# Performance work log

Hardware: AMD Instinct MI355X
Metric: run time of the kernel (lower is better)

The kernel has to match this reference:

```python
import jax, jax.numpy as jnp
import numpy as np

N = 50_000      # nodes
E = 800_000     # edges
IN_NF = 16      # input/output node feature dim
H = 64          # hidden_nf
NB = 2          # n_layers (EquivariantBlocks)
NG = 2          # inv_sublayers (GCLs per block)
NORM_FACTOR = 100.0
NORM_CONST = 1.0
EDGE_IN = 2 * H + 2  # edges_in_d = 2 (current + initial squared distance)


def setup_inputs() -> dict:
    key = jax.random.key(0)
    ks = iter(jax.random.split(key, 32))
    rn = lambda s: jax.random.normal(next(ks), s, dtype=jnp.float32)
    lin = lambda s: rn(s) / np.sqrt(s[-2]).astype(np.float32)  # ~xavier-ish
    inp = {
        'h': rn((N, IN_NF)),
        'x': rn((N, 3)),
        'row': jax.random.randint(next(ks), (E,), 0, N, dtype=jnp.int32),
        'col': jax.random.randint(next(ks), (E,), 0, N, dtype=jnp.int32),
        # embedding in/out
        'emb_w': lin((IN_NF, H)), 'emb_b': jnp.zeros((H,), jnp.float32),
        'out_w': lin((H, IN_NF)), 'out_b': jnp.zeros((IN_NF,), jnp.float32),
        # 4 GCLs total (NB*NG), stacked on leading axis
        'e_w1': lin((NB * NG, EDGE_IN, H)), 'e_b1': jnp.zeros((NB * NG, H), jnp.float32),
        'e_w2': lin((NB * NG, H, H)),       'e_b2': jnp.zeros((NB * NG, H), jnp.float32),
        'n_w1': lin((NB * NG, 2 * H, H)),   'n_b1': jnp.zeros((NB * NG, H), jnp.float32),
        'n_w2': lin((NB * NG, H, H)),       'n_b2': jnp.zeros((NB * NG, H), jnp.float32),
        # 2 EquivariantUpdates (one per block)
        'q_w1': lin((NB, EDGE_IN, H)), 'q_b1': jnp.zeros((NB, H), jnp.float32),
        'q_w2': lin((NB, H, H)),       'q_b2': jnp.zeros((NB, H), jnp.float32),
        'q_w3': lin((NB, H, 1)) * 0.001,  # xavier gain=0.001, no bias
    }
    return inp


def _egnn(h, x, row, col, emb_w, emb_b, out_w, out_b,
          e_w1, e_b1, e_w2, e_b2, n_w1, n_b1, n_w2, n_b2,
          q_w1, q_b1, q_w2, q_b2, q_w3):
    def coord2diff(xc):
        d = xc[row] - xc[col]                      # [E,3]
        radial = jnp.sum(d * d, axis=1, keepdims=True)  # [E,1]
        d = d / (jnp.sqrt(radial + 1e-8) + NORM_CONST)
        return radial, d

    dist0, _ = coord2diff(x)                       # initial distances, passed to every block
    h = h @ emb_w + emb_b
    for b in range(NB):
        radial, coord_diff = coord2diff(x)
        edge_attr = jnp.concatenate([radial, dist0], axis=1)  # [E,2]
        for i in range(NG):
            l = b * NG + i
            inp = jnp.concatenate([h[row], h[col], edge_attr], axis=1)  # [E, 2H+2]
            mij = jax.nn.silu(jax.nn.silu(inp @ e_w1[l] + e_b1[l]) @ e_w2[l] + e_b2[l])
            agg = jax.ops.segment_sum(mij, row, num_segments=N) / NORM_FACTOR
            node_in = jnp.concatenate([h, agg], axis=1)                 # [N, 2H]
            h = h + jax.nn.silu(node_in @ n_w1[l] + n_b1[l]) @ n_w2[l] + n_b2[l]
        # equivariant coordinate update
        inp = jnp.concatenate([h[row], h[col], edge_attr], axis=1)
        phi = jax.nn.silu(jax.nn.silu(inp @ q_w1[b] + q_b1[b]) @ q_w2[b] + q_b2[b]) @ q_w3[b]  # [E,1]
        trans = coord_diff * phi
        x = x + jax.ops.segment_sum(trans, row, num_segments=N) / NORM_FACTOR
    h = h @ out_w + out_b
    return h, x


def reference(h, x, row, col, emb_w, emb_b, out_w, out_b,
              e_w1, e_b1, e_w2, e_b2, n_w1, n_b1, n_w2, n_b2,
              q_w1, q_b1, q_w2, q_b2, q_w3):
    return _egnn(h, x, row, col, emb_w, emb_b, out_w, out_b,
                 e_w1, e_b1, e_w2, e_b2, n_w1, n_b1, n_w2, n_b2,
                 q_w1, q_b1, q_w2, q_b2, q_w3)
```

## Files before the change

kernel.cpp:

```cpp
#include <hip/hip_runtime.h>

#define NN 50000
#define NE 800000
#define NB 196

typedef unsigned int  u32;
typedef unsigned short u16;
typedef __attribute__((ext_vector_type(8))) short short8;
typedef __attribute__((ext_vector_type(4))) float f32x4;

union ABfrag { uint2 u2[2]; uint4 u4; short8 s8; };

__device__ __forceinline__ float silu_f(float v) {
    return v * __builtin_amdgcn_rcpf(1.0f + __expf(-v));
}
__device__ __forceinline__ u32 pk2(float lo, float hi) {
    return __builtin_amdgcn_perm(__float_as_uint(hi) + 0x8000u,
                                 __float_as_uint(lo) + 0x8000u, 0x07060302u);
}
__device__ __forceinline__ float bff(u32 h) { return __uint_as_float(h << 16); }

__global__ __launch_bounds__(256, 4) void k_embed(const float* __restrict__ h,
        const float* __restrict__ w, const float* __restrict__ b,
        float* __restrict__ h64) {
    int n = blockIdx.x * 256 + threadIdx.x;
    if (n >= NN) return;
    const float4* h4 = (const float4*)(h + (long)n * 16);
    float in[16];
    #pragma unroll
    for (int c = 0; c < 4; ++c) {
        float4 v = h4[c];
        in[4*c+0] = v.x; in[4*c+1] = v.y; in[4*c+2] = v.z; in[4*c+3] = v.w;
    }
    float acc[64];
    #pragma unroll
    for (int j = 0; j < 64; ++j) acc[j] = b[j];
    #pragma unroll
    for (int k = 0; k < 16; ++k) {
        #pragma unroll
        for (int j = 0; j < 64; ++j) acc[j] = fmaf(in[k], w[k*64 + j], acc[j]);
    }
    float4* o4 = (float4*)(h64 + (long)n * 64);
    #pragma unroll
    for (int c = 0; c < 16; ++c)
        o4[c] = make_float4(acc[4*c+0], acc[4*c+1], acc[4*c+2], acc[4*c+3]);
}

__global__ __launch_bounds__(256, 4) void k_hist(const int* __restrict__ row,
        int* __restrict__ deg) {
    int e = blockIdx.x * 256 + threadIdx.x;
    if (e < NE) atomicAdd(&deg[row[e]], 1);
}

__global__ __launch_bounds__(256, 4) void k_scanA(const int* __restrict__ deg,
        int* __restrict__ bsum) {
    int t = threadIdx.x, i = blockIdx.x * 256 + t;
    int v = (i < NN) ? deg[i] : 0;
    #pragma unroll
    for (int d = 1; d < 64; d <<= 1) v += __shfl_xor(v, d);
    __shared__ int ws[4];
    if ((t & 63) == 0) ws[t >> 6] = v;
    __syncthreads();
    if (t == 0) bsum[blockIdx.x] = ws[0] + ws[1] + ws[2] + ws[3];
}

__global__ __launch_bounds__(256) void k_scanB(const int* __restrict__ bsum,
        int* __restrict__ bpre) {
    __shared__ int s[256];
    int t = threadIdx.x;
    int v = (t < NB) ? bsum[t] : 0;
    s[t] = v;
    __syncthreads();
    #pragma unroll
    for (int d = 1; d < 256; d <<= 1) {
        int u = (t >= d) ? s[t - d] : 0;
        __syncthreads();
        s[t] += u;
        __syncthreads();
    }
    if (t < NB) bpre[t] = s[t] - v;
}

__global__ __launch_bounds__(256, 4) void k_scanC(const int* __restrict__ deg,
        const int* __restrict__ bpre, int* __restrict__ base) {
    int t = threadIdx.x, i = blockIdx.x * 256 + t;
    int lane = t & 63, w = t >> 6;
    int v = (i < NN) ? deg[i] : 0;
    int x = v;
    #pragma unroll
    for (int d = 1; d < 64; d <<= 1) {
        int u = __shfl_up(x, d);
        if (lane >= d) x += u;
    }
    __shared__ int wsum[4];
    if (lane == 63) wsum[w] = x;
    __syncthreads();
    int off = bpre[blockIdx.x];
    #pragma unroll
    for (int ww = 0; ww < 3; ++ww) if (ww < w) off += wsum[ww];
    if (i < NN) base[i] = off + x - v;
}

__global__ __launch_bounds__(256, 4) void k_scatter(const int* __restrict__ row,
        const int* __restrict__ col, int* __restrict__ base,
        int* __restrict__ rowS, int* __restrict__ colS) {
    int e = blockIdx.x * 256 + threadIdx.x;
    if (e >= NE) return;
    int r = row[e];
    int p = atomicAdd(&base[r], 1);
    rowS[p] = r;
    colS[p] = col[e];
}

__global__ __launch_bounds__(256, 4) void k_radial(const float* __restrict__ x,
        const int* __restrict__ rowS, const int* __restrict__ colS,
        float* __restrict__ radial) {
    int e = blockIdx.x * 256 + threadIdx.x;
    if (e >= NE) return;
    int r = rowS[e], c = colS[e];
    float dx = x[r*3+0] - x[c*3+0];
    float dy = x[r*3+1] - x[c*3+1];
    float dz = x[r*3+2] - x[c*3+2];
    radial[e] = dx*dx + dy*dy + dz*dz;
}

__device__ __forceinline__ u32 bfr_rne(float x) {
    u32 u = __float_as_uint(x);
    u += 0x7fffu + ((u >> 16) & 1u);
    return u >> 16;
}
__global__ __launch_bounds__(256, 4) void k_wconv(const float* __restrict__ e_w2,
        const float* __restrict__ q_w2, const float* __restrict__ n_w1,
        const float* __restrict__ n_w2, const float* __restrict__ e_w1,
        const float* __restrict__ q_w1, u16* __restrict__ wf) {
    int t = blockIdx.x * 256 + threadIdx.x;
    if (t >= 122880) return;
    int j, lane, n, s, k, col;
    if (t < 24576) {
        int L = t >> 12, v = t & 4095;
        j = v & 7; lane = (v >> 3) & 63; int ns = v >> 9; n = ns >> 1; s = ns & 1;
        k = 8*(lane >> 4) + j + 32*s;
        col = 16*n + (lane & 15);
        const float* src = (L < 4) ? e_w2 + (size_t)L*4096 : q_w2 + (size_t)(L-4)*4096;
        wf[t] = (u16)bfr_rne(src[k*64 + col]);
    } else if (t < 57344) {
        int u = t - 24576; int L = u >> 13, v = u & 8191;
        j = v & 7; lane = (v >> 3) & 63; int ns = v >> 9; n = ns >> 2; s = ns & 3;
        k = 8*(lane >> 4) + j + 32*s;
        col = 16*n + (lane & 15);
        wf[t] = (u16)bfr_rne(n_w1[(size_t)L*8192 + k*64 + col]);
    } else if (t < 73728) {
        int u = t - 57344; int L = u >> 12, v = u & 4095;
        j = v & 7; lane = (v >> 3) & 63; int ns = v >> 9; n = ns >> 1; s = ns & 1;
        k = 8*(lane >> 4) + j + 32*s;
        col = 16*n + (lane & 15);
        wf[t] = (u16)bfr_rne(n_w2[(size_t)L*4096 + k*64 + col]);
    } else {
        int u = t - 73728;
        int L = u >> 13;
        int v = u & 8191;
        int m = v >> 12;
        int v2 = v & 4095;
        j = v2 & 7; lane = (v2 >> 3) & 63; int ns = v2 >> 9; n = ns >> 1; s = ns & 1;
        k = 8*(lane >> 4) + j + 32*s;
        col = 16*n + (lane & 15);
        const float* src = (L < 4) ? e_w1 + (size_t)L*130*64
                                   : q_w1 + (size_t)(L-4)*130*64;
        wf[t] = (u16)bfr_rne(src[(size_t)(m*64 + k)*64 + col]);
    }
}

__global__ __launch_bounds__(256, 4) void k_pq(const float* __restrict__ h64,
        const u16* __restrict__ wpf, const float* __restrict__ b1,
        u32* __restrict__ Pb, u32* __restrict__ Qb) {
    __shared__ u16 A[64*64];
    __shared__ u16 XP[64*68], XQ[64*68];
    int t = threadIdx.x, w = t >> 6, lane = t & 63;
    int nb0 = blockIdx.x * 64;
    #pragma unroll
    for (int i = 0; i < 4; ++i) {
        int idx = i*256 + t;
        int r = idx >> 4, c = idx & 15;
        int n = nb0 + r;
        float4 v = make_float4(0.f, 0.f, 0.f, 0.f);
        if (n < NN) v = ((const float4*)(h64 + (size_t)n*64))[c];
        uint2 pk = make_uint2(pk2(v.x, v.y), pk2(v.z, v.w));
        *(uint2*)((char*)A + r*128 + ((8*c) ^ ((r & 15) << 3))) = pk;
    }
    __syncthreads();
    int r0 = lane & 15, g = lane >> 4;
    ABfrag bp[2], bq[2];
    #pragma unroll
    for (int s = 0; s < 2; ++s) {
        bp[s].u4 = *(const uint4*)(wpf + ((size_t)(w*2 + s)*64 + lane)*8);
        bq[s].u4 = *(const uint4*)(wpf + 4096 + ((size_t)(w*2 + s)*64 + lane)*8);
    }
    f32x4 aP[4], aQ[4];
    #pragma unroll
    for (int t4 = 0; t4 < 4; ++t4) {
        aP[t4] = (f32x4){0.f, 0.f, 0.f, 0.f};
        aQ[t4] = (f32x4){0.f, 0.f, 0.f, 0.f};
    }
    #pragma unroll
    for (int t4 = 0; t4 < 4; ++t4) {
        #pragma unroll
        for (int s = 0; s < 2; ++s) {
            int boff = 16*g + 64*s;
            ABfrag af;
            af.u2[0] = *(uint2*)((char*)A + (16*t4 + r0)*128 + ( boff      ^ (r0 << 3)));
            af.u2[1] = *(uint2*)((char*)A + (16*t4 + r0)*128 + ((boff + 8) ^ (r0 << 3)));
            aP[t4] = __builtin_amdgcn_mfma_f32_16x16x32_bf16(af.s8, bp[s].s8, aP[t4], 0, 0, 0);
            aQ[t4] = __builtin_amdgcn_mfma_f32_16x16x32_bf16(af.s8, bq[s].s8, aQ[t4], 0, 0, 0);
        }
    }
    float bv = b1[16*w + r0];
    #pragma unroll
    for (int t4 = 0; t4 < 4; ++t4)
        #pragma unroll
        for (int q = 0; q < 4; ++q) {
            int rw = 16*t4 + 4*g + q;
            XP[rw*68 + 16*w + r0] = (u16)(pk2(aP[t4][q] + bv, 0.f) & 0xffffu);
            XQ[rw*68 + 16*w + r0] = (u16)(pk2(aQ[t4][q], 0.f) & 0xffffu);
        }
    __syncthreads();
    int node = t >> 2, part = t & 3;
    if (nb0 + node < NN) {
        const u32* XPw = (const u32*)XP;
        const u32* XQw = (const u32*)XQ;
        u32 b[8];
        #pragma unroll
        for (int j = 0; j < 8; ++j) b[j] = XPw[node*34 + 8*part + j];
        uint4* dp = (uint4*)(Pb + (size_t)(nb0 + node)*32 + part*8);
        dp[0] = make_uint4(b[0], b[1], b[2], b[3]);
        dp[1] = make_uint4(b[4], b[5], b[6], b[7]);
        #pragma unroll
        for (int j = 0; j < 8; ++j) b[j] = XQw[node*34 + 8*part + j];
        uint4* dq = (uint4*)(Qb + (size_t)(nb0 + node)*32 + part*8);
        dq[0] = make_uint4(b[0], b[1], b[2], b[3]);
        dq[1] = make_uint4(b[4], b[5], b[6], b[7]);
    }
}

__global__ __launch_bounds__(256, 4) void k_edge(
        const u32* __restrict__ Pb, const u32* __restrict__ Qb,
        const float* __restrict__ radial, const float* __restrict__ dist0,
        const int* __restrict__ rowS, const int* __restrict__ colS,
        const float* __restrict__ w1t, const u16* __restrict__ w2f,
        const float* __restrict__ b2, float* __restrict__ agg) {
    __shared__ u16 M_lds[4][64*66];
    int tid = threadIdx.x;
    int w = tid >> 6, lane = tid & 63;
    int ebase = blockIdx.x * 256 + w * 64;
    u16* Mw = M_lds[w];
    int r0 = lane & 15, g = lane >> 4;
    float wa[16], wb[16];
    *(float4*)&wa[0]  = *(const float4*)(w1t + 8*g);
    *(float4*)&wa[4]  = *(const float4*)(w1t + 8*g + 4);
    *(float4*)&wa[8]  = *(const float4*)(w1t + 32 + 8*g);
    *(float4*)&wa[12] = *(const float4*)(w1t + 36 + 8*g);
    *(float4*)&wb[0]  = *(const float4*)(w1t + 64 + 8*g);
    *(float4*)&wb[4]  = *(const float4*)(w1t + 68 + 8*g);
    *(float4*)&wb[8]  = *(const float4*)(w1t + 96 + 8*g);
    *(float4*)&wb[12] = *(const float4*)(w1t + 100 + 8*g);
    ABfrag bf[4][2];
    #pragma unroll
    for (int n = 0; n < 4; ++n)
        #pragma unroll
        for (int s = 0; s < 2; ++s)
            bf[n][s].u4 = *(const uint4*)(w2f + ((n*2 + s)*64 + lane)*8);
    float b2v[4];
    #pragma unroll
    for (int n = 0; n < 4; ++n) b2v[n] = b2[16*n + r0];
    #pragma unroll
    for (int t = 0; t < 4; ++t) {
        int et = ebase + 16*t + r0;
        int r = rowS[et], c = colS[et];
        float rad = radial[et], d0 = dist0[et];
        uint4 pA = *(const uint4*)(Pb + (size_t)r*32 + 4*g);
        uint4 pB = *(const uint4*)(Pb + (size_t)r*32 + 16 + 4*g);
        uint4 qA = *(const uint4*)(Qb + (size_t)c*32 + 4*g);
        uint4 qB = *(const uint4*)(Qb + (size_t)c*32 + 16 + 4*g);
        u32 pu[8] = {pA.x, pA.y, pA.z, pA.w, pB.x, pB.y, pB.z, pB.w};
        u32 qu[8] = {qA.x, qA.y, qA.z, qA.w, qB.x, qB.y, qB.z, qB.w};
        u32 pk[8];
        #pragma unroll
        for (int i = 0; i < 8; ++i) {
            int kb = (i >> 2) * 8 + (i & 3) * 2;
            float pl = bff(pu[i] & 0xffffu), ph = bff(pu[i] >> 16);
            float ql = bff(qu[i] & 0xffffu), qh = bff(qu[i] >> 16);
            float h0 = silu_f(pl + ql + rad*wa[kb]   + d0*wb[kb]);
            float h1 = silu_f(ph + qh + rad*wa[kb+1] + d0*wb[kb+1]);
            pk[i] = pk2(h0, h1);
        }
        ABfrag af0, af1;
        af0.u4 = make_uint4(pk[0], pk[1], pk[2], pk[3]);
        af1.u4 = make_uint4(pk[4], pk[5], pk[6], pk[7]);
        f32x4 acc[4];
        #pragma unroll
        for (int n = 0; n < 4; ++n) acc[n] = (f32x4){0.f, 0.f, 0.f, 0.f};
        #pragma unroll
        for (int n = 0; n < 4; ++n) {
            acc[n] = __builtin_amdgcn_mfma_f32_16x16x32_bf16(af0.s8, bf[n][0].s8, acc[n], 0, 0, 0);
            acc[n] = __builtin_amdgcn_mfma_f32_16x16x32_bf16(af1.s8, bf[n][1].s8, acc[n], 0, 0, 0);
        }
        #pragma unroll
        for (int n = 0; n < 4; ++n) {
            f32x4 z = acc[n];
            u32 m0 = pk2(silu_f(z[0] + b2v[n]), silu_f(z[1] + b2v[n]));
            u32 m1 = pk2(silu_f(z[2] + b2v[n]), silu_f(z[3] + b2v[n]));
            *(uint2*)((char*)Mw + (16*n + r0)*132 + 32*t + 8*g) = make_uint2(m0, m1);
        }
    }
    int rl = rowS[ebase + lane];
    int rnext = __shfl_down(rl, 1);
    unsigned long long tm = __ballot((lane == 63) || (rnext != rl));
    float racc = 0.0f;
    #pragma unroll
    for (int ch = 0; ch < 16; ++ch) {
        uint2 mm = *(uint2*)((char*)Mw + lane*132 + 8*ch);
        u32 mw[2] = {mm.x, mm.y};
        #pragma unroll
        for (int q = 0; q < 4; ++q) {
            int ee = 4*ch + q;
            racc += bff((mw[q >> 1] >> ((q & 1) * 16)) & 0xffffu);
            if ((tm >> ee) & 1ull) {
                int rr = __builtin_amdgcn_readlane(rl, ee);
                atomicAdd(&agg[(size_t)rr*64 + lane], racc);
                racc = 0.0f;
            }
        }
    }
}

__global__ __launch_bounds__(256, 3) void k_node_pq(float* __restrict__ h64,
        const float* __restrict__ agg,
        const u16* __restrict__ w1f, const float* __restrict__ b1,
        const u16* __restrict__ w2f, const float* __restrict__ b2,
        const u16* __restrict__ wpf, const float* __restrict__ b1pq,
        u32* __restrict__ Pb, u32* __restrict__ Qb) {
    __shared__ u16 S[16512];
    u16* A0 = S;
    u16* A1 = S + 4096;
    u16* H  = S + 8192;
    u16* D  = S + 12288;
    u16* An = S;
    u16* XPh = S + 4096;
    u16* XQh = S + 8448;
    int t = threadIdx.x, w = t >> 6, lane = t & 63;
    int nb0 = blockIdx.x * 64;
    #pragma unroll
    for (int i = 0; i < 8; ++i) {
        int idx = i*256 + t;
        int r = idx >> 5, c = idx & 31;
        int n = nb0 + r;
        float4 v = make_float4(0.f, 0.f, 0.f, 0.f);
        if (n < NN) {
            if (c < 16) v = ((const float4*)(h64 + (size_t)n*64))[c];
            else {
                float4 a = ((const float4*)(agg + (size_t)n*64))[c-16];
                v = make_float4(a.x*0.01f, a.y*0.01f, a.z*0.01f, a.w*0.01f);
            }
        }
        uint2 pk = make_uint2(pk2(v.x, v.y), pk2(v.z, v.w));
        u16* dst = (c < 16) ? A0 : A1;
        int cc = c & 15;
        *(uint2*)((char*)dst + r*128 + ((8*cc) ^ ((r & 15) << 3))) = pk;
    }
    __syncthreads();
    int r0 = lane & 15, g = lane >> 4;
    ABfrag bf1[4];
    #pragma unroll
    for (int s = 0; s < 4; ++s)
        bf1[s].u4 = *(const uint4*)(w1f + ((size_t)(w*4 + s)*64 + lane)*8);
    f32x4 acc[4];
    #pragma unroll
    for (int t4 = 0; t4 < 4; ++t4) acc[t4] = (f32x4){0.f, 0.f, 0.f, 0.f};
    #pragma unroll
    for (int t4 = 0; t4 < 4; ++t4) {
        #pragma unroll
        for (int s = 0; s < 4; ++s) {
            const u16* Ah = (s < 2) ? A0 : A1;
            int boff = 16*g + 64*(s & 1);
            ABfrag af;
            af.u2[0] = *(uint2*)((char*)Ah + (16*t4 + r0)*128 + ( boff      ^ (r0 << 3)));
            af.u2[1] = *(uint2*)((char*)Ah + (16*t4 + r0)*128 + ((boff + 8) ^ (r0 << 3)));
            acc[t4] = __builtin_amdgcn_mfma_f32_16x16x32_bf16(
                af.s8, bf1[s].s8, acc[t4], 0, 0, 0);
        }
    }
    float b1v = b1[16*w + r0];
    #pragma unroll
    for (int t4 = 0; t4 < 4; ++t4)
        #pragma unroll
        for (int q = 0; q < 4; ++q) {
            int rw = 16*t4 + 4*g + q;
            u16 hv = (u16)(pk2(silu_f(acc[t4][q] + b1v), 0.f) & 0xffffu);
            *(u16*)((char*)H + rw*128 + ((2*(16*w + r0)) ^ ((rw & 15) << 3))) = hv;
        }
    __syncthreads();
    ABfrag bf2[2];
    #pragma unroll
    for (int s = 0; s < 2; ++s)
        bf2[s].u4 = *(const uint4*)(w2f + ((size_t)(w*2 + s)*64 + lane)*8);
    f32x4 acc2[4];
    #pragma unroll
    for (int t4 = 0; t4 < 4; ++t4) acc2[t4] = (f32x4){0.f, 0.f, 0.f, 0.f};
    #pragma unroll
    for (int t4 = 0; t4 < 4; ++t4) {
        #pragma unroll
        for (int s = 0; s < 2; ++s) {
            int boff = 16*g + 64*s;
            ABfrag af;
            af.u2[0] = *(uint2*)((char*)H + (16*t4 + r0)*128 + ( boff      ^ (r0 << 3)));
            af.u2[1] = *(uint2*)((char*)H + (16*t4 + r0)*128 + ((boff + 8) ^ (r0 << 3)));
            acc2[t4] = __builtin_amdgcn_mfma_f32_16x16x32_bf16(
                af.s8, bf2[s].s8, acc2[t4], 0, 0, 0);
        }
    }
    float b2v = b2[16*w + r0];
    #pragma unroll
    for (int t4 = 0; t4 < 4; ++t4)
        #pragma unroll
        for (int q = 0; q < 4; ++q) {
            int rw = 16*t4 + 4*g + q;
            D[rw*66 + 16*w + r0] = (u16)(pk2(acc2[t4][q] + b2v, 0.f) & 0xffffu);
        }
    __syncthreads();
    #pragma unroll
    for (int i = 0; i < 4; ++i) {
        int idx = i*256 + t;
        int rr = idx >> 4, cc = idx & 15;
        int n = nb0 + rr;
        float4 v = make_float4(0.f, 0.f, 0.f, 0.f);
        if (n < NN) {
            v = ((const float4*)(h64 + (size_t)n*64))[cc];
            v.x += bff(D[rr*66 + 4*cc + 0]);
            v.y += bff(D[rr*66 + 4*cc + 1]);
            v.z += bff(D[rr*66 + 4*cc + 2]);
            v.w += bff(D[rr*66 + 4*cc + 3]);
            ((float4*)(h64 + (size_t)n*64))[cc] = v;
        }
        uint2 pk = make_uint2(pk2(v.x, v.y), pk2(v.z, v.w));
        *(uint2*)((char*)An + rr*128 + ((8*cc) ^ ((rr & 15) << 3))) = pk;
    }
    __syncthreads();
    ABfrag bp[2], bq[2];
    #pragma unroll
    for (int s = 0; s < 2; ++s) {
        bp[s].u4 = *(const uint4*)(wpf + ((size_t)(w*2 + s)*64 + lane)*8);
        bq[s].u4 = *(const uint4*)(wpf + 4096 + ((size_t)(w*2 + s)*64 + lane)*8);
    }
    f32x4 aP[4], aQ[4];
    #pragma unroll
    for (int t4 = 0; t4 < 4; ++t4) {
        aP[t4] = (f32x4){0.f, 0.f, 0.f, 0.f};
        aQ[t4] = (f32x4){0.f, 0.f, 0.f, 0.f};
    }
    #pragma unroll
    for (int t4 = 0; t4 < 4; ++t4) {
        #pragma unroll
        for (int s = 0; s < 2; ++s) {
            int boff = 16*g + 64*s;
            ABfrag af;
            af.u2[0] = *(uint2*)((char*)An + (16*t4 + r0)*128 + ( boff      ^ (r0 << 3)));
            af.u2[1] = *(uint2*)((char*)An + (16*t4 + r0)*128 + ((boff + 8) ^ (r0 << 3)));
            aP[t4] = __builtin_amdgcn_mfma_f32_16x16x32_bf16(af.s8, bp[s].s8, aP[t4], 0, 0, 0);
            aQ[t4] = __builtin_amdgcn_mfma_f32_16x16x32_bf16(af.s8, bq[s].s8, aQ[t4], 0, 0, 0);
        }
    }
    float bv = b1pq[16*w + r0];
    #pragma unroll
    for (int t4 = 0; t4 < 4; ++t4)
        #pragma unroll
        for (int q = 0; q < 4; ++q) {
            int rw = 16*t4 + 4*g + q;
            XPh[rw*68 + 16*w + r0] = (u16)(pk2(aP[t4][q] + bv, 0.f) & 0xffffu);
            XQh[rw*68 + 16*w + r0] = (u16)(pk2(aQ[t4][q], 0.f) & 0xffffu);
        }
    __syncthreads();
    int node = t >> 2, part = t & 3;
    if (nb0 + node < NN) {
        const u32* XPw = (const u32*)XPh;
        const u32* XQw = (const u32*)XQh;
        u32 b[8];
        #pragma unroll
        for (int j = 0; j < 8; ++j) b[j] = XPw[node*34 + 8*part + j];
        uint4* dp = (uint4*)(Pb + (size_t)(nb0 + node)*32 + part*8);
        dp[0] = make_uint4(b[0], b[1], b[2], b[3]);
        dp[1] = make_uint4(b[4], b[5], b[6], b[7]);
        #pragma unroll
        for (int j = 0; j < 8; ++j) b[j] = XQw[node*34 + 8*part + j];
        uint4* dq = (uint4*)(Qb + (size_t)(nb0 + node)*32 + part*8);
        dq[0] = make_uint4(b[0], b[1], b[2], b[3]);
        dq[1] = make_uint4(b[4], b[5], b[6], b[7]);
    }
}

__global__ __launch_bounds__(256, 4) void k_coord(
        const u32* __restrict__ Pb, const u32* __restrict__ Qb,
        const float* __restrict__ radial, const float* __restrict__ dist0,
        const int* __restrict__ rowS, const int* __restrict__ colS,
        const float* __restrict__ w1t, const u16* __restrict__ w2f,
        const float* __restrict__ b2, const float* __restrict__ w3,
        const float* __restrict__ x_old, float* __restrict__ x_new) {
    __shared__ float PHL[4][64];
    int tid = threadIdx.x;
    int w = tid >> 6, lane = tid & 63;
    int ebase = blockIdx.x * 256 + w * 64;
    int r0 = lane & 15, g = lane >> 4;
    float wa[16], wb[16];
    *(float4*)&wa[0]  = *(const float4*)(w1t + 8*g);
    *(float4*)&wa[4]  = *(const float4*)(w1t + 8*g + 4);
    *(float4*)&wa[8]  = *(const float4*)(w1t + 32 + 8*g);
    *(float4*)&wa[12] = *(const float4*)(w1t + 36 + 8*g);
    *(float4*)&wb[0]  = *(const float4*)(w1t + 64 + 8*g);
    *(float4*)&wb[4]  = *(const float4*)(w1t + 68 + 8*g);
    *(float4*)&wb[8]  = *(const float4*)(w1t + 96 + 8*g);
    *(float4*)&wb[12] = *(const float4*)(w1t + 100 + 8*g);
    ABfrag bf[4][2];
    #pragma unroll
    for (int n = 0; n < 4; ++n)
        #pragma unroll
        for (int s = 0; s < 2; ++s)
            bf[n][s].u4 = *(const uint4*)(w2f + ((n*2 + s)*64 + lane)*8);
    float w3v[4], b2v[4];
    #pragma unroll
    for (int n = 0; n < 4; ++n) { w3v[n] = w3[16*n + r0]; b2v[n] = b2[16*n + r0]; }
    float ph[16];
    #pragma unroll
    for (int t = 0; t < 4; ++t) {
        int et = ebase + 16*t + r0;
        int r = rowS[et], c = colS[et];
        float rad = radial[et], d0 = dist0[et];
        uint4 pA = *(const uint4*)(Pb + (size_t)r*32 + 4*g);
        uint4 pB = *(const uint4*)(Pb + (size_t)r*32 + 16 + 4*g);
        uint4 qA = *(const uint4*)(Qb + (size_t)c*32 + 4*g);
        uint4 qB = *(const uint4*)(Qb + (size_t)c*32 + 16 + 4*g);
        u32 pu[8] = {pA.x, pA.y, pA.z, pA.w, pB.x, pB.y, pB.z, pB.w};
        u32 qu[8] = {qA.x, qA.y, qA.z, qA.w, qB.x, qB.y, qB.z, qB.w};
        u32 pk[8];
        #pragma unroll
        for (int i = 0; i < 8; ++i) {
            int kb = (i >> 2) * 8 + (i & 3) * 2;
            float pl = bff(pu[i] & 0xffffu), phh = bff(pu[i] >> 16);
            float ql = bff(qu[i] & 0xffffu), qh = bff(qu[i] >> 16);
            float h0 = silu_f(pl + ql + rad*wa[kb]   + d0*wb[kb]);
            float h1 = silu_f(phh + qh + rad*wa[kb+1] + d0*wb[kb+1]);
            pk[i] = pk2(h0, h1);
        }
        ABfrag af0, af1;
        af0.u4 = make_uint4(pk[0], pk[1], pk[2], pk[3]);
        af1.u4 = make_uint4(pk[4], pk[5], pk[6], pk[7]);
        f32x4 acc[4];
        #pragma unroll
        for (int n = 0; n < 4; ++n) acc[n] = (f32x4){0.f, 0.f, 0.f, 0.f};
        #pragma unroll
        for (int n = 0; n < 4; ++n) {
            acc[n] = __builtin_amdgcn_mfma_f32_16x16x32_bf16(af0.s8, bf[n][0].s8, acc[n], 0, 0, 0);
            acc[n] = __builtin_amdgcn_mfma_f32_16x16x32_bf16(af1.s8, bf[n][1].s8, acc[n], 0, 0, 0);
        }
        #pragma unroll
        for (int q = 0; q < 4; ++q) {
            float s = 0.f;
            #pragma unroll
            for (int n = 0; n < 4; ++n)
                s = fmaf(silu_f(acc[n][q] + b2v[n]), w3v[n], s);
            ph[t*4 + q] = s;
        }
    }
    #pragma unroll
    for (int d = 1; d < 16; d <<= 1)
        #pragma unroll
        for (int i = 0; i < 16; ++i) ph[i] += __shfl_xor(ph[i], d);
    if (r0 == 0) {
        #pragma unroll
        for (int t = 0; t < 4; ++t)
            #pragma unroll
            for (int q = 0; q < 4; ++q)
                PHL[w][16*t + 4*g + q] = ph[t*4 + q];
    }
    int e = ebase + lane;
    float phi = PHL[w][lane] * 0.01f;
    int r = rowS[e], c = colS[e];
    float rad = radial[e];
    float dx = x_old[r*3+0] - x_old[c*3+0];
    float dy = x_old[r*3+1] - x_old[c*3+1];
    float dz = x_old[r*3+2] - x_old[c*3+2];
    float inv = phi / (sqrtf(rad + 1e-8f) + 1.0f);
    float tx = dx * inv, ty = dy * inv, tz = dz * inv;
    int rprev = __shfl_up(r, 1);
    bool head = (lane == 0) || (rprev != r);
    unsigned long long hm = __ballot(head);
    int runid = __popcll(hm & ((2ull << lane) - 1ull));
    #pragma unroll
    for (int d = 1; d < 64; d <<= 1) {
        float ox = __shfl_up(tx, d);
        float oy = __shfl_up(ty, d);
        float oz = __shfl_up(tz, d);
        int orid = __shfl_up(runid, d);
        if (lane >= d && orid == runid) { tx += ox; ty += oy; tz += oz; }
    }
    int rid_next = __shfl_down(runid, 1);
    bool tail = (lane == 63) || (rid_next != runid);
    if (tail) {
        atomicAdd(&x_new[r*3+0], tx);
        atomicAdd(&x_new[r*3+1], ty);
        atomicAdd(&x_new[r*3+2], tz);
    }
}

__global__ __launch_bounds__(256, 4) void k_out(const float* __restrict__ h64,
        const float* __restrict__ w, const float* __restrict__ b,
        float* __restrict__ out) {
    int n = blockIdx.x * 256 + threadIdx.x;
    if (n >= NN) return;
    float acc[16];
    #pragma unroll
    for (int j = 0; j < 16; ++j) acc[j] = b[j];
    const float4* h4 = (const float4*)(h64 + (long)n*64);
    #pragma unroll
    for (int c = 0; c < 16; ++c) {
        float4 v = h4[c];
        float vv[4] = {v.x, v.y, v.z, v.w};
        #pragma unroll
        for (int t = 0; t < 4; ++t) {
            #pragma unroll
            for (int j = 0; j < 16; ++j)
                acc[j] = fmaf(vv[t], w[(4*c+t)*16 + j], acc[j]);
        }
    }
    float4* o4 = (float4*)(out + (long)n*16);
    #pragma unroll
    for (int cq = 0; cq < 4; ++cq)
        o4[cq] = make_float4(acc[4*cq+0],acc[4*cq+1],acc[4*cq+2],acc[4*cq+3]);
}

extern "C" void kernel_launch(void* const* d_in, const int* in_sizes, int n_in,
                              void* d_out, int out_size, void* d_ws, size_t ws_size,
                              hipStream_t stream) {
    const float* h_in  = (const float*)d_in[0];
    const float* x_in  = (const float*)d_in[1];
    const int*   row   = (const int*)d_in[2];
    const int*   col   = (const int*)d_in[3];
    const float* emb_w = (const float*)d_in[4];
    const float* emb_b = (const float*)d_in[5];
    const float* out_w = (const float*)d_in[6];
    const float* out_b = (const float*)d_in[7];
    const float* e_w1  = (const float*)d_in[8];
    const float* e_b1  = (const float*)d_in[9];
    const float* e_w2  = (const float*)d_in[10];
    const float* e_b2  = (const float*)d_in[11];
    const float* n_w1  = (const float*)d_in[12];
    const float* n_b1  = (const float*)d_in[13];
    const float* n_w2  = (const float*)d_in[14];
    const float* n_b2  = (const float*)d_in[15];
    const float* q_w1  = (const float*)d_in[16];
    const float* q_b1  = (const float*)d_in[17];
    const float* q_w2  = (const float*)d_in[18];
    const float* q_b2  = (const float*)d_in[19];
    const float* q_w3  = (const float*)d_in[20];

    const size_t WF_N = 122880;
    const size_t WF_BYTES = WF_N * sizeof(u16);
    size_t need = WF_BYTES + ((size_t)NN*64*4 + (size_t)NE*2 + (size_t)NN*3
                   + (size_t)NE*2 + (size_t)NN*2 + 1024) * sizeof(float);
    if (ws_size < need) return;

    u16*   wf    = (u16*)d_ws;
    float* fb    = (float*)((char*)d_ws + WF_BYTES);
    float* h64   = fb;
    u32*   Pb    = (u32*)(h64 + (size_t)NN*64);
    u32*   Qb    = Pb + (size_t)NN*32;
    float* agg   = (float*)(Qb + (size_t)NN*32);
    float* d0S   = agg   + (size_t)NN*64;
    float* radS  = d0S   + (size_t)NE;
    float* xA    = radS  + (size_t)NE;
    int*   rowS  = (int*)(xA + (size_t)NN*3);
    int*   colS  = rowS  + (size_t)NE;
    int*   deg   = colS  + (size_t)NE;
    int*   base  = deg   + (size_t)NN;
    int*   bsum  = base  + (size_t)NN;
    int*   bpre  = bsum  + 256;

    float* out_h = (float*)d_out;
    float* out_x = out_h + (size_t)NN*16;

    dim3 th(256);
    dim3 nb((NN + 255)/256);
    dim3 eb(NE/256);
    dim3 t64b((NN + 63)/64);

    hipMemsetAsync(deg, 0, (size_t)NN*sizeof(int), stream);
    k_hist<<<eb, th, 0, stream>>>(row, deg);
    k_scanA<<<NB, th, 0, stream>>>(deg, bsum);
    k_scanB<<<1, th, 0, stream>>>(bsum, bpre);
    k_scanC<<<NB, th, 0, stream>>>(deg, bpre, base);
    k_scatter<<<eb, th, 0, stream>>>(row, col, base, rowS, colS);
    k_wconv<<<480, th, 0, stream>>>(e_w2, q_w2, n_w1, n_w2, e_w1, q_w1, wf);

    k_radial<<<eb, th, 0, stream>>>(x_in, rowS, colS, d0S);
    k_embed<<<nb, th, 0, stream>>>(h_in, emb_w, emb_b, h64);

    const u16* nw1f = wf + 24576;
    const u16* nw2f = wf + 57344;
    const u16* pqf  = wf + 73728;

    for (int b = 0; b < 2; ++b) {
        const float* x_old;
        float*       x_new;
        const float* radp;
        if (b == 0) {
            x_old = x_in;  x_new = xA;    radp = d0S;
        } else {
            x_old = xA;    x_new = out_x; radp = radS;
            k_radial<<<eb, th, 0, stream>>>(x_old, rowS, colS, radS);
        }
        for (int i = 0; i < 2; ++i) {
            int l = b*2 + i;
            if (i == 0)
                k_pq<<<t64b, th, 0, stream>>>(h64, pqf + (size_t)l*8192,
                                              e_b1 + (size_t)l*64, Pb, Qb);
            hipMemsetAsync(agg, 0, (size_t)NN*64*sizeof(float), stream);
            k_edge<<<eb, th, 0, stream>>>(Pb, Qb, radp, d0S, rowS, colS,
                    e_w1 + (size_t)l*130*64 + 128*64,
                    wf + (size_t)l*4096,
                    e_b2 + (size_t)l*64, agg);
            const u16* nxt_f  = (i == 0) ? pqf + (size_t)(l+1)*8192
                                         : pqf + (size_t)(4 + b)*8192;
            const float* nxt_b = (i == 0) ? e_b1 + (size_t)(l+1)*64
                                          : q_b1 + (size_t)b*64;
            k_node_pq<<<t64b, th, 0, stream>>>(h64, agg,
                    nw1f + (size_t)l*8192, n_b1 + (size_t)l*64,
                    nw2f + (size_t)l*4096, n_b2 + (size_t)l*64,
                    nxt_f, nxt_b, Pb, Qb);
        }
        hipMemcpyAsync(x_new, x_old, (size_t)NN*3*sizeof(float),
                       hipMemcpyDeviceToDevice, stream);
        k_coord<<<eb, th, 0, stream>>>(Pb, Qb, radp, d0S, rowS, colS,
                q_w1 + (size_t)b*130*64 + 128*64,
                wf + (size_t)(4 + b)*4096,
                q_b2 + (size_t)b*64, q_w3 + (size_t)b*64, x_old, x_new);
    }
    k_out<<<nb, th, 0, stream>>>(h64, out_w, out_b, out_h);
}
```

Before: 668.8 us.

## Pack edge records, zero agg in node kernel, fuse next block's PQ projection

Edge row, col, initial distance and current radial are packed into one int4 record per sorted edge, so edge and coord kernels issue a single 16-byte load instead of four scalar loads. The node kernel now zeroes agg after reading it, which removes the per-layer memset. The last node kernel of block 0 also computes the P/Q projections for block 1's first GCL into a second buffer, which removes a separate k_pq launch. The host loop is unrolled explicitly, and the cost is extra workspace for the second P/Q buffers plus the unused padding in each edge record.

```diff
diff --git a/kernel.cpp b/kernel.cpp
--- a/kernel.cpp
+++ b/kernel.cpp
@@ -103,25 +103,27 @@
 
 __global__ __launch_bounds__(256, 4) void k_scatter(const int* __restrict__ row,
         const int* __restrict__ col, int* __restrict__ base,
-        int* __restrict__ rowS, int* __restrict__ colS) {
+        int4* __restrict__ erec) {
     int e = blockIdx.x * 256 + threadIdx.x;
     if (e >= NE) return;
     int r = row[e];
     int p = atomicAdd(&base[r], 1);
-    rowS[p] = r;
-    colS[p] = col[e];
+    erec[p] = make_int4(r, col[e], 0, 0);
 }
 
 __global__ __launch_bounds__(256, 4) void k_radial(const float* __restrict__ x,
-        const int* __restrict__ rowS, const int* __restrict__ colS,
-        float* __restrict__ radial) {
+        int4* __restrict__ erec, int mode) {
     int e = blockIdx.x * 256 + threadIdx.x;
     if (e >= NE) return;
-    int r = rowS[e], c = colS[e];
+    int4 rec = erec[e];
+    int r = rec.x, c = rec.y;
     float dx = x[r*3+0] - x[c*3+0];
     float dy = x[r*3+1] - x[c*3+1];
     float dz = x[r*3+2] - x[c*3+2];
-    radial[e] = dx*dx + dy*dy + dz*dz;
+    float rad = dx*dx + dy*dy + dz*dz;
+    rec.w = __float_as_int(rad);
+    if (mode == 0) rec.z = rec.w;
+    erec[e] = rec;
 }
 
 __device__ __forceinline__ u32 bfr_rne(float x) {
@@ -243,8 +245,7 @@
 
 __global__ __launch_bounds__(256, 4) void k_edge(
         const u32* __restrict__ Pb, const u32* __restrict__ Qb,
-        const float* __restrict__ radial, const float* __restrict__ dist0,
-        const int* __restrict__ rowS, const int* __restrict__ colS,
+        const int4* __restrict__ erec,
         const float* __restrict__ w1t, const u16* __restrict__ w2f,
         const float* __restrict__ b2, float* __restrict__ agg) {
     __shared__ u16 M_lds[4][64*66];
@@ -274,8 +275,9 @@
     #pragma unroll
     for (int t = 0; t < 4; ++t) {
         int et = ebase + 16*t + r0;
-        int r = rowS[et], c = colS[et];
-        float rad = radial[et], d0 = dist0[et];
+        int4 rec = erec[et];
+        int r = rec.x, c = rec.y;
+        float d0 = __int_as_float(rec.z), rad = __int_as_float(rec.w);
         uint4 pA = *(const uint4*)(Pb + (size_t)r*32 + 4*g);
         uint4 pB = *(const uint4*)(Pb + (size_t)r*32 + 16 + 4*g);
         uint4 qA = *(const uint4*)(Qb + (size_t)c*32 + 4*g);
@@ -311,7 +313,7 @@
             *(uint2*)((char*)Mw + (16*n + r0)*132 + 32*t + 8*g) = make_uint2(m0, m1);
         }
     }
-    int rl = rowS[ebase + lane];
+    int rl = *(const int*)(erec + ebase + lane);
     int rnext = __shfl_down(rl, 1);
     unsigned long long tm = __ballot((lane == 63) || (rnext != rl));
     float racc = 0.0f;
@@ -333,11 +335,13 @@
 }
 
 __global__ __launch_bounds__(256, 3) void k_node_pq(float* __restrict__ h64,
-        const float* __restrict__ agg,
+        float* __restrict__ agg,
         const u16* __restrict__ w1f, const float* __restrict__ b1,
         const u16* __restrict__ w2f, const float* __restrict__ b2,
         const u16* __restrict__ wpf, const float* __restrict__ b1pq,
-        u32* __restrict__ Pb, u32* __restrict__ Qb) {
+        u32* __restrict__ Pb, u32* __restrict__ Qb,
+        const u16* __restrict__ wpf2, const float* __restrict__ b1pq2,
+        u32* __restrict__ Pb2, u32* __restrict__ Qb2, int has2) {
     __shared__ u16 S[16512];
     u16* A0 = S;
     u16* A1 = S + 4096;
@@ -358,6 +362,7 @@
             if (c < 16) v = ((const float4*)(h64 + (size_t)n*64))[c];
             else {
                 float4 a = ((const float4*)(agg + (size_t)n*64))[c-16];
+                ((float4*)(agg + (size_t)n*64))[c-16] = make_float4(0.f,0.f,0.f,0.f);
                 v = make_float4(a.x*0.01f, a.y*0.01f, a.z*0.01f, a.w*0.01f);
             }
         }
@@ -444,62 +449,68 @@
         *(uint2*)((char*)An + rr*128 + ((8*cc) ^ ((rr & 15) << 3))) = pk;
     }
     __syncthreads();
-    ABfrag bp[2], bq[2];
-    #pragma unroll
-    for (int s = 0; s < 2; ++s) {
-        bp[s].u4 = *(const uint4*)(wpf + ((size_t)(w*2 + s)*64 + lane)*8);
-        bq[s].u4 = *(const uint4*)(wpf + 4096 + ((size_t)(w*2 + s)*64 + lane)*8);
-    }
-    f32x4 aP[4], aQ[4];
-    #pragma unroll
-    for (int t4 = 0; t4 < 4; ++t4) {
-        aP[t4] = (f32x4){0.f, 0.f, 0.f, 0.f};
-        aQ[t4] = (f32x4){0.f, 0.f, 0.f, 0.f};
-    }
-    #pragma unroll
-    for (int t4 = 0; t4 < 4; ++t4) {
+    for (int set = 0; set < 1 + (has2 ? 1 : 0); ++set) {
+        const u16* wp = set ? wpf2 : wpf;
+        const float* bb = set ? b1pq2 : b1pq;
+        u32* Pd = set ? Pb2 : Pb;
+        u32* Qd = set ? Qb2 : Qb;
+        ABfrag bp[2], bq[2];
         #pragma unroll
         for (int s = 0; s < 2; ++s) {
-            int boff = 16*g + 64*s;
-            ABfrag af;
-            af.u2[0] = *(uint2*)((char*)An + (16*t4 + r0)*128 + ( boff      ^ (r0 << 3)));
-            af.u2[1] = *(uint2*)((char*)An + (16*t4 + r0)*128 + ((boff + 8) ^ (r0 << 3)));
-            aP[t4] = __builtin_amdgcn_mfma_f32_16x16x32_bf16(af.s8, bp[s].s8, aP[t4], 0, 0, 0);
-            aQ[t4] = __builtin_amdgcn_mfma_f32_16x16x32_bf16(af.s8, bq[s].s8, aQ[t4], 0, 0, 0);
-        }
-    }
-    float bv = b1pq[16*w + r0];
-    #pragma unroll
-    for (int t4 = 0; t4 < 4; ++t4)
-        #pragma unroll
-        for (int q = 0; q < 4; ++q) {
-            int rw = 16*t4 + 4*g + q;
-            XPh[rw*68 + 16*w + r0] = (u16)(pk2(aP[t4][q] + bv, 0.f) & 0xffffu);
-            XQh[rw*68 + 16*w + r0] = (u16)(pk2(aQ[t4][q], 0.f) & 0xffffu);
-        }
-    __syncthreads();
-    int node = t >> 2, part = t & 3;
-    if (nb0 + node < NN) {
-        const u32* XPw = (const u32*)XPh;
-        const u32* XQw = (const u32*)XQh;
-        u32 b[8];
-        #pragma unroll
-        for (int j = 0; j < 8; ++j) b[j] = XPw[node*34 + 8*part + j];
-        uint4* dp = (uint4*)(Pb + (size_t)(nb0 + node)*32 + part*8);
-        dp[0] = make_uint4(b[0], b[1], b[2], b[3]);
-        dp[1] = make_uint4(b[4], b[5], b[6], b[7]);
-        #pragma unroll
-        for (int j = 0; j < 8; ++j) b[j] = XQw[node*34 + 8*part + j];
-        uint4* dq = (uint4*)(Qb + (size_t)(nb0 + node)*32 + part*8);
-        dq[0] = make_uint4(b[0], b[1], b[2], b[3]);
-        dq[1] = make_uint4(b[4], b[5], b[6], b[7]);
+            bp[s].u4 = *(const uint4*)(wp + ((size_t)(w*2 + s)*64 + lane)*8);
+            bq[s].u4 = *(const uint4*)(wp + 4096 + ((size_t)(w*2 + s)*64 + lane)*8);
+        }
+        f32x4 aP[4], aQ[4];
+        #pragma unroll
+        for (int t4 = 0; t4 < 4; ++t4) {
+            aP[t4] = (f32x4){0.f, 0.f, 0.f, 0.f};
+            aQ[t4] = (f32x4){0.f, 0.f, 0.f, 0.f};
+        }
+        #pragma unroll
+        for (int t4 = 0; t4 < 4; ++t4) {
+            #pragma unroll
+            for (int s = 0; s < 2; ++s) {
+                int boff = 16*g + 64*s;
+                ABfrag af;
+                af.u2[0] = *(uint2*)((char*)An + (16*t4 + r0)*128 + ( boff      ^ (r0 << 3)));
+                af.u2[1] = *(uint2*)((char*)An + (16*t4 + r0)*128 + ((boff + 8) ^ (r0 << 3)));
+                aP[t4] = __builtin_amdgcn_mfma_f32_16x16x32_bf16(af.s8, bp[s].s8, aP[t4], 0, 0, 0);
+                aQ[t4] = __builtin_amdgcn_mfma_f32_16x16x32_bf16(af.s8, bq[s].s8, aQ[t4], 0, 0, 0);
+            }
+        }
+        float bv = bb[16*w + r0];
+        #pragma unroll
+        for (int t4 = 0; t4 < 4; ++t4)
+            #pragma unroll
+            for (int q = 0; q < 4; ++q) {
+                int rw = 16*t4 + 4*g + q;
+                XPh[rw*68 + 16*w + r0] = (u16)(pk2(aP[t4][q] + bv, 0.f) & 0xffffu);
+                XQh[rw*68 + 16*w + r0] = (u16)(pk2(aQ[t4][q], 0.f) & 0xffffu);
+            }
+        __syncthreads();
+        int node = t >> 2, part = t & 3;
+        if (nb0 + node < NN) {
+            const u32* XPw = (const u32*)XPh;
+            const u32* XQw = (const u32*)XQh;
+            u32 b[8];
+            #pragma unroll
+            for (int j = 0; j < 8; ++j) b[j] = XPw[node*34 + 8*part + j];
+            uint4* dp = (uint4*)(Pd + (size_t)(nb0 + node)*32 + part*8);
+            dp[0] = make_uint4(b[0], b[1], b[2], b[3]);
+            dp[1] = make_uint4(b[4], b[5], b[6], b[7]);
+            #pragma unroll
+            for (int j = 0; j < 8; ++j) b[j] = XQw[node*34 + 8*part + j];
+            uint4* dq = (uint4*)(Qd + (size_t)(nb0 + node)*32 + part*8);
+            dq[0] = make_uint4(b[0], b[1], b[2], b[3]);
+            dq[1] = make_uint4(b[4], b[5], b[6], b[7]);
+        }
+        __syncthreads();
     }
 }
 
 __global__ __launch_bounds__(256, 4) void k_coord(
         const u32* __restrict__ Pb, const u32* __restrict__ Qb,
-        const float* __restrict__ radial, const float* __restrict__ dist0,
-        const int* __restrict__ rowS, const int* __restrict__ colS,
+        const int4* __restrict__ erec,
         const float* __restrict__ w1t, const u16* __restrict__ w2f,
         const float* __restrict__ b2, const float* __restrict__ w3,
         const float* __restrict__ x_old, float* __restrict__ x_new) {
@@ -530,8 +541,9 @@
     #pragma unroll
     for (int t = 0; t < 4; ++t) {
         int et = ebase + 16*t + r0;
-        int r = rowS[et], c = colS[et];
-        float rad = radial[et], d0 = dist0[et];
+        int4 rec = erec[et];
+        int r = rec.x, c = rec.y;
+        float d0 = __int_as_float(rec.z), rad = __int_as_float(rec.w);
         uint4 pA = *(const uint4*)(Pb + (size_t)r*32 + 4*g);
         uint4 pB = *(const uint4*)(Pb + (size_t)r*32 + 16 + 4*g);
         uint4 qA = *(const uint4*)(Qb + (size_t)c*32 + 4*g);
@@ -581,8 +593,9 @@
     }
     int e = ebase + lane;
     float phi = PHL[w][lane] * 0.01f;
-    int r = rowS[e], c = colS[e];
-    float rad = radial[e];
+    int4 rec = erec[e];
+    int r = rec.x, c = rec.y;
+    float rad = __int_as_float(rec.w);
     float dx = x_old[r*3+0] - x_old[c*3+0];
     float dy = x_old[r*3+1] - x_old[c*3+1];
     float dz = x_old[r*3+2] - x_old[c*3+2];
@@ -662,25 +675,24 @@
 
     const size_t WF_N = 122880;
     const size_t WF_BYTES = WF_N * sizeof(u16);
-    size_t need = WF_BYTES + ((size_t)NN*64*4 + (size_t)NE*2 + (size_t)NN*3
-                   + (size_t)NE*2 + (size_t)NN*2 + 1024) * sizeof(float);
+    size_t need = WF_BYTES + ((size_t)NN*64 + (size_t)NN*32*4 + (size_t)NN*64
+                   + (size_t)NE*4 + (size_t)NN*3 + (size_t)NN*2 + 2048) * 4;
     if (ws_size < need) return;
 
     u16*   wf    = (u16*)d_ws;
     float* fb    = (float*)((char*)d_ws + WF_BYTES);
     float* h64   = fb;
     u32*   Pb    = (u32*)(h64 + (size_t)NN*64);
-    u32*   Qb    = Pb + (size_t)NN*32;
-    float* agg   = (float*)(Qb + (size_t)NN*32);
-    float* d0S   = agg   + (size_t)NN*64;
-    float* radS  = d0S   + (size_t)NE;
-    float* xA    = radS  + (size_t)NE;
-    int*   rowS  = (int*)(xA + (size_t)NN*3);
-    int*   colS  = rowS  + (size_t)NE;
-    int*   deg   = colS  + (size_t)NE;
-    int*   base  = deg   + (size_t)NN;
-    int*   bsum  = base  + (size_t)NN;
-    int*   bpre  = bsum  + 256;
+    u32*   Qb    = Pb  + (size_t)NN*32;
+    u32*   Pb2   = Qb  + (size_t)NN*32;
+    u32*   Qb2   = Pb2 + (size_t)NN*32;
+    float* agg   = (float*)(Qb2 + (size_t)NN*32);
+    int4*  erec  = (int4*)(agg + (size_t)NN*64);
+    float* xA    = (float*)(erec + (size_t)NE);
+    int*   deg   = (int*)(xA + (size_t)NN*3);
+    int*   base  = deg  + (size_t)NN;
+    int*   bsum  = base + (size_t)NN;
+    int*   bpre  = bsum + 256;
 
     float* out_h = (float*)d_out;
     float* out_x = out_h + (size_t)NN*16;
@@ -695,51 +707,55 @@
     k_scanA<<<NB, th, 0, stream>>>(deg, bsum);
     k_scanB<<<1, th, 0, stream>>>(bsum, bpre);
     k_scanC<<<NB, th, 0, stream>>>(deg, bpre, base);
-    k_scatter<<<eb, th, 0, stream>>>(row, col, base, rowS, colS);
+    k_scatter<<<eb, th, 0, stream>>>(row, col, base, erec);
     k_wconv<<<480, th, 0, stream>>>(e_w2, q_w2, n_w1, n_w2, e_w1, q_w1, wf);
 
-    k_radial<<<eb, th, 0, stream>>>(x_in, rowS, colS, d0S);
+    k_radial<<<eb, th, 0, stream>>>(x_in, erec, 0);
     k_embed<<<nb, th, 0, stream>>>(h_in, emb_w, emb_b, h64);
+    hipMemsetAsync(agg, 0, (size_t)NN*64*sizeof(float), stream);
 
     const u16* nw1f = wf + 24576;
     const u16* nw2f = wf + 57344;
     const u16* pqf  = wf + 73728;
 
-    for (int b = 0; b < 2; ++b) {
-        const float* x_old;
-        float*       x_new;
-        const float* radp;
-        if (b == 0) {
-            x_old = x_in;  x_new = xA;    radp = d0S;
-        } else {
-            x_old = xA;    x_new = out_x; radp = radS;
-            k_radial<<<eb, th, 0, stream>>>(x_old, rowS, colS, radS);
-        }
-        for (int i = 0; i < 2; ++i) {
-            int l = b*2 + i;
-            if (i == 0)
-                k_pq<<<t64b, th, 0, stream>>>(h64, pqf + (size_t)l*8192,
-                                              e_b1 + (size_t)l*64, Pb, Qb);
-            hipMemsetAsync(agg, 0, (size_t)NN*64*sizeof(float), stream);
-            k_edge<<<eb, th, 0, stream>>>(Pb, Qb, radp, d0S, rowS, colS,
-                    e_w1 + (size_t)l*130*64 + 128*64,
-                    wf + (size_t)l*4096,
-                    e_b2 + (size_t)l*64, agg);
-            const u16* nxt_f  = (i == 0) ? pqf + (size_t)(l+1)*8192
-                                         : pqf + (size_t)(4 + b)*8192;
-            const float* nxt_b = (i == 0) ? e_b1 + (size_t)(l+1)*64
-                                          : q_b1 + (size_t)b*64;
-            k_node_pq<<<t64b, th, 0, stream>>>(h64, agg,
-                    nw1f + (size_t)l*8192, n_b1 + (size_t)l*64,
-                    nw2f + (size_t)l*4096, n_b2 + (size_t)l*64,
-                    nxt_f, nxt_b, Pb, Qb);
-        }
-        hipMemcpyAsync(x_new, x_old, (size_t)NN*3*sizeof(float),
-                       hipMemcpyDeviceToDevice, stream);
-        k_coord<<<eb, th, 0, stream>>>(Pb, Qb, radp, d0S, rowS, colS,
-                q_w1 + (size_t)b*130*64 + 128*64,
-                wf + (size_t)(4 + b)*4096,
-                q_b2 + (size_t)b*64, q_w3 + (size_t)b*64, x_old, x_new);
-    }
+    k_pq<<<t64b, th, 0, stream>>>(h64, pqf, e_b1, Pb, Qb);
+    k_edge<<<eb, th, 0, stream>>>(Pb, Qb, erec,
+            e_w1 + 128*64, wf, e_b2, agg);
+    k_node_pq<<<t64b, th, 0, stream>>>(h64, agg,
+            nw1f, n_b1, nw2f, n_b2,
+            pqf + 8192, e_b1 + 64, Pb, Qb,
+            nullptr, nullptr, nullptr, nullptr, 0);
+    k_edge<<<eb, th, 0, stream>>>(Pb, Qb, erec,
+            e_w1 + (size_t)1*130*64 + 128*64, wf + 4096, e_b2 + 64, agg);
+    k_node_pq<<<t64b, th, 0, stream>>>(h64, agg,
+            nw1f + 8192, n_b1 + 64, nw2f + 4096, n_b2 + 64,
+            pqf + (size_t)4*8192, q_b1, Pb, Qb,
+            pqf + (size_t)2*8192, e_b1 + 128, Pb2, Qb2, 1);
+    hipMemcpyAsync(xA, x_in, (size_t)NN*3*sizeof(float),
+                   hipMemcpyDeviceToDevice, stream);
+    k_coord<<<eb, th, 0, stream>>>(Pb, Qb, erec,
+            q_w1 + 128*64, wf + (size_t)4*4096, q_b2, q_w3, x_in, xA);
+
+    k_radial<<<eb, th, 0, stream>>>(xA, erec, 1);
+    k_edge<<<eb, th, 0, stream>>>(Pb2, Qb2, erec,
+            e_w1 + (size_t)2*130*64 + 128*64, wf + (size_t)2*4096,
+            e_b2 + 128, agg);
+    k_node_pq<<<t64b, th, 0, stream>>>(h64, agg,
+            nw1f + (size_t)2*8192, n_b1 + 128, nw2f + (size_t)2*4096, n_b2 + 128,
+            pqf + (size_t)3*8192, e_b1 + 192, Pb, Qb,
+            nullptr, nullptr, nullptr, nullptr, 0);
+    k_edge<<<eb, th, 0, stream>>>(Pb, Qb, erec,
+            e_w1 + (size_t)3*130*64 + 128*64, wf + (size_t)3*4096,
+            e_b2 + 192, agg);
+    k_node_pq<<<t64b, th, 0, stream>>>(h64, agg,
+            nw1f + (size_t)3*8192, n_b1 + 192, nw2f + (size_t)3*4096, n_b2 + 192,
+            pqf + (size_t)5*8192, q_b1 + 64, Pb, Qb,
+            nullptr, nullptr, nullptr, nullptr, 0);
+    hipMemcpyAsync(out_x, xA, (size_t)NN*3*sizeof(float),
+                   hipMemcpyDeviceToDevice, stream);
+    k_coord<<<eb, th, 0, stream>>>(Pb, Qb, erec,
+            q_w1 + (size_t)1*130*64 + 128*64, wf + (size_t)5*4096,
+            q_b2 + 64, q_w3 + 64, xA, out_x);
+
     k_out<<<nb, th, 0, stream>>>(h64, out_w, out_b, out_h);
 }
```

New measurement: 668.0 us. Within noise of the previous version (-0.1%).
